# Performance work log

Hardware: AMD Instinct MI355X
Metric: run time of the kernel (lower is better)

## Reference

```python
import jax, jax.numpy as jnp
import numpy as np

NUM_RELATIONS = 8


def rgcn_conv(x, edge_index, edge_type, W, root, bias):
    """PyG RGCNConv (full weights, aggr='mean'): for each relation r, mean-aggregate
    W_r @ x_src over incoming edges of type r at each target node, sum over relations,
    then add root transform and bias."""
    N = x.shape[0]
    src, dst = edge_index[0], edge_index[1]
    # per-(relation, dst) edge counts for mean aggregation
    comb = edge_type * N + dst  # [E]
    cnt = jax.ops.segment_sum(jnp.ones(src.shape[0], x.dtype), comb,
                              num_segments=NUM_RELATIONS * N)  # [R*N]
    inv = jnp.where(cnt > 0, 1.0 / cnt, 0.0)
    # per-relation transformed features [R, N, H]
    xW = jnp.einsum('ni,rio->rno', x, W)
    # per-edge message, pre-scaled by 1/count for mean aggregation
    msg = xW[edge_type, src] * inv[comb][:, None]  # [E, H]
    agg = jax.ops.segment_sum(msg, dst, num_segments=N)  # [N, H]
    return agg + x @ root + bias


def setup_inputs() -> dict:
    key = jax.random.key(0)
    ks = jax.random.split(key, 9)
    N, E, D, H, C, R = 50000, 600000, 128, 128, 16, NUM_RELATIONS
    s1 = 1.0 / np.sqrt(D)
    s2 = 1.0 / np.sqrt(H)
    return {
        'x': jax.random.normal(ks[0], (N, D), jnp.float32),
        'edge_index': jax.random.randint(ks[1], (2, E), 0, N, jnp.int32),
        'edge_type': jax.random.randint(ks[2], (E,), 0, R, jnp.int32),
        'W1': jax.random.normal(ks[3], (R, D, H), jnp.float32) * s1,
        'root1': jax.random.normal(ks[4], (D, H), jnp.float32) * s1,
        'b1': jnp.zeros((H,), jnp.float32),
        'W2': jax.random.normal(ks[5], (R, H, H), jnp.float32) * s2,
        'root2': jax.random.normal(ks[6], (H, H), jnp.float32) * s2,
        'b2': jnp.zeros((H,), jnp.float32),
        'Wc': jax.random.normal(ks[7], (H, C), jnp.float32) * s2,
        'bc': jnp.zeros((C,), jnp.float32),
    }


def reference(x, edge_index, edge_type, W1, root1, b1, W2, root2, b2, Wc, bc):
    h = jax.nn.relu(rgcn_conv(x, edge_index, edge_type, W1, root1, b1))
    # dropout(p=0.2) is identity in eval mode
    embeddings = rgcn_conv(h, edge_index, edge_type, W2, root2, b2)
    out = embeddings @ Wc + bc
    return (out, embeddings)
```

## Files before the change

kernel.cpp:

```cpp
#include <hip/hip_runtime.h>

#define NREL 8

typedef __attribute__((ext_vector_type(8))) short bf16x8;
typedef __attribute__((ext_vector_type(4))) float f32x4;

__device__ inline ushort f2bf(float f)
{
    union { float f; unsigned u; } v; v.f = f;
    unsigned r = v.u + 0x7FFF + ((v.u >> 16) & 1);
    return (ushort)(r >> 16);
}

__device__ inline unsigned cvtpk(float lo, float hi)
{
    unsigned r;
    asm("v_cvt_pk_bf16_f32 %0, %1, %2" : "=v"(r) : "v"(lo), "v"(hi));
    return r;
}

__global__ __launch_bounds__(256) void zero16(float4* __restrict__ p, int n4)
{
    int i = blockIdx.x * 256 + threadIdx.x;
    int stride = gridDim.x * 256;
    for (; i < n4; i += stride) p[i] = make_float4(0.f, 0.f, 0.f, 0.f);
}

__global__ __launch_bounds__(256) void count_edges(
    const int* __restrict__ ei, const int* __restrict__ et,
    int* __restrict__ cnt, int E, int N)
{
    int e = blockIdx.x * 256 + threadIdx.x;
    if (e < E) {
        int d = ei[E + e];
        int r = et[e];
        atomicAdd(&cnt[r * N + d], 1);
    }
}

__global__ __launch_bounds__(256) void scan1f(
    const int* __restrict__ cnt, float* __restrict__ invc8,
    int* __restrict__ part, int* __restrict__ bsum, int N)
{
    __shared__ int tmp[256];
    int d = blockIdx.x * 256 + threadIdx.x;
    int s = 0;
    if (d < N) {
        #pragma unroll
        for (int r = 0; r < NREL; r++) {
            int c = cnt[r * N + d];
            s += c;
            invc8[(size_t)d * 8 + r] = (c > 0) ? 1.f / (float)c : 0.f;
        }
    }
    int v = s;
    tmp[threadIdx.x] = v;
    __syncthreads();
    for (int off = 1; off < 256; off <<= 1) {
        int t = (threadIdx.x >= off) ? tmp[threadIdx.x - off] : 0;
        __syncthreads();
        tmp[threadIdx.x] += t;
        __syncthreads();
    }
    if (d < N) part[d] = tmp[threadIdx.x] - v;
    if (threadIdx.x == 255) bsum[blockIdx.x] = tmp[255];
}

__global__ __launch_bounds__(1024) void scan2(int* __restrict__ bsum, int nb)
{
    __shared__ int tmp[1024];
    int tid = threadIdx.x;
    int v = (tid < nb) ? bsum[tid] : 0;
    tmp[tid] = v;
    __syncthreads();
    for (int off = 1; off < 1024; off <<= 1) {
        int t = (tid >= off) ? tmp[tid - off] : 0;
        __syncthreads();
        tmp[tid] += t;
        __syncthreads();
    }
    if (tid < nb) bsum[tid] = tmp[tid] - v;
}

__global__ __launch_bounds__(256) void scan3(
    const int* __restrict__ part, const int* __restrict__ bsum,
    int* __restrict__ rowptr, int* __restrict__ cursor, int n, int E)
{
    int i = blockIdx.x * 256 + threadIdx.x;
    if (i < n) {
        int v = part[i] + bsum[blockIdx.x];
        rowptr[i] = v;
        cursor[i] = v;
    }
    if (i == 0) rowptr[n] = E;
}

__global__ __launch_bounds__(256) void fill_csr(
    const int* __restrict__ ei, const int* __restrict__ et,
    int* __restrict__ cursor, int* __restrict__ spk, int E)
{
    int e = blockIdx.x * 256 + threadIdx.x;
    if (e < E) {
        int d = ei[E + e];
        int pos = atomicAdd(&cursor[d], 1);
        spk[pos] = (ei[e] << 8) | et[e];
    }
}

__global__ __launch_bounds__(256) void conv_x(
    const float* __restrict__ x, ushort* __restrict__ xb, int n4)
{
    int i = blockIdx.x * 256 + threadIdx.x;
    int stride = gridDim.x * 256;
    for (; i < n4; i += stride) {
        float4 v = ((const float4*)x)[i];
        ushort4 o;
        o.x = f2bf(v.x); o.y = f2bf(v.y); o.z = f2bf(v.z); o.w = f2bf(v.w);
        ((ushort4*)xb)[i] = o;
    }
}

__global__ __launch_bounds__(256) void conv_wfB(
    const float* __restrict__ W1, const float* __restrict__ root1,
    ushort* __restrict__ Wf1,
    const float* __restrict__ W2, const float* __restrict__ root2,
    ushort* __restrict__ Wf2)
{
    const float* W    = blockIdx.y ? W2 : W1;
    const float* root = blockIdx.y ? root2 : root1;
    ushort* Wf        = blockIdx.y ? Wf2 : Wf1;
    int i = blockIdx.x * 256 + threadIdx.x;
    if (i >= 128 * 1152) return;
    int f = i >> 9;
    int within = i & 511;
    int l = within >> 3;
    int j = within & 7;
    int rs = f >> 5;
    int kk = (f >> 3) & 3;
    int n  = f & 7;
    int col = (n << 4) | (l & 15);
    int kl  = kk * 32 + (l >> 4) * 8 + j;
    float v = (rs < 8) ? W[rs * 16384 + kl * 128 + col] : root[kl * 128 + col];
    Wf[i] = f2bf(v);
}

__global__ __launch_bounds__(1024, 8) void fused_layer(
    const ushort* __restrict__ Xb, const int* __restrict__ rowptr,
    const int* __restrict__ spk, const float* __restrict__ invc8,
    const ushort* __restrict__ Wf, const float* __restrict__ bias,
    float* __restrict__ Ofp, ushort* __restrict__ Obf, int N, int relu)
{
    __shared__ ushort lds[8 * 32 * 128];
    __shared__ f32x4 pscr[2][512];

    int wid  = threadIdx.x >> 6;
    int lane = threadIdx.x & 63;
    int blk0 = blockIdx.x * 32;
    int lane4 = lane << 2;

    #pragma unroll 1
    for (int rr = 0; rr < 2; rr++) {
        int lrow32 = wid * 2 + rr;
        int d = blk0 + lrow32;

        float2 a0 = {0.f, 0.f}, a1 = {0.f, 0.f}, a2 = {0.f, 0.f}, a3 = {0.f, 0.f};
        float2 a4 = {0.f, 0.f}, a5 = {0.f, 0.f}, a6 = {0.f, 0.f}, a7 = {0.f, 0.f};

        #define ROWLD(SP) \
            (*(const unsigned*)((const char*)Xb + (unsigned)((SP) | lane4)))
        #define CONSUME(P, U)                                               \
        {                                                                   \
            union { unsigned u; float f; } lo, hi;                          \
            lo.u = (U) << 16; hi.u = (U) & 0xFFFF0000u;                     \
            switch ((P) & 0xFF) {                                           \
                case 0: a0.x += lo.f; a0.y += hi.f; break;                  \
                case 1: a1.x += lo.f; a1.y += hi.f; break;                  \
                case 2: a2.x += lo.f; a2.y += hi.f; break;                  \
                case 3: a3.x += lo.f; a3.y += hi.f; break;                  \
                case 4: a4.x += lo.f; a4.y += hi.f; break;                  \
                case 5: a5.x += lo.f; a5.y += hi.f; break;                  \
                case 6: a6.x += lo.f; a6.y += hi.f; break;                  \
                default: a7.x += lo.f; a7.y += hi.f; break;                 \
            }                                                               \
        }

        if (d < N) {
            int beg = rowptr[d], end = rowptr[d + 1];
            int i = beg;
            for (; i + 8 <= end; i += 8) {
                int pk8 = spk[i + (lane & 7)];
                int p0 = __builtin_amdgcn_readlane(pk8, 0);
                int p1 = __builtin_amdgcn_readlane(pk8, 1);
                int p2 = __builtin_amdgcn_readlane(pk8, 2);
                int p3 = __builtin_amdgcn_readlane(pk8, 3);
                int p4 = __builtin_amdgcn_readlane(pk8, 4);
                int p5 = __builtin_amdgcn_readlane(pk8, 5);
                int p6 = __builtin_amdgcn_readlane(pk8, 6);
                int p7 = __builtin_amdgcn_readlane(pk8, 7);
                unsigned u0 = ROWLD(p0 & 0xFFFFFF00);
                unsigned u1 = ROWLD(p1 & 0xFFFFFF00);
                unsigned u2 = ROWLD(p2 & 0xFFFFFF00);
                unsigned u3 = ROWLD(p3 & 0xFFFFFF00);
                unsigned u4 = ROWLD(p4 & 0xFFFFFF00);
                unsigned u5 = ROWLD(p5 & 0xFFFFFF00);
                unsigned u6 = ROWLD(p6 & 0xFFFFFF00);
                unsigned u7 = ROWLD(p7 & 0xFFFFFF00);
                CONSUME(p0, u0);
                CONSUME(p1, u1);
                CONSUME(p2, u2);
                CONSUME(p3, u3);
                CONSUME(p4, u4);
                CONSUME(p5, u5);
                CONSUME(p6, u6);
                CONSUME(p7, u7);
            }
            for (; i + 4 <= end; i += 4) {
                int pk4 = spk[i + (lane & 3)];
                int p0 = __builtin_amdgcn_readlane(pk4, 0);
                int p1 = __builtin_amdgcn_readlane(pk4, 1);
                int p2 = __builtin_amdgcn_readlane(pk4, 2);
                int p3 = __builtin_amdgcn_readlane(pk4, 3);
                unsigned u0 = ROWLD(p0 & 0xFFFFFF00);
                unsigned u1 = ROWLD(p1 & 0xFFFFFF00);
                unsigned u2 = ROWLD(p2 & 0xFFFFFF00);
                unsigned u3 = ROWLD(p3 & 0xFFFFFF00);
                CONSUME(p0, u0);
                CONSUME(p1, u1);
                CONSUME(p2, u2);
                CONSUME(p3, u3);
            }
            for (; i < end; i++) {
                int p = __builtin_amdgcn_readfirstlane(spk[i]);
                unsigned u = ROWLD(p & 0xFFFFFF00);
                CONSUME(p, u);
            }
        }
        #undef CONSUME
        #undef ROWLD

        f32x4 iv0 = {0.f, 0.f, 0.f, 0.f}, iv1 = {0.f, 0.f, 0.f, 0.f};
        if (d < N) {
            iv0 = *(const f32x4*)&invc8[(size_t)d * 8];
            iv1 = *(const f32x4*)&invc8[(size_t)d * 8 + 4];
        }
        unsigned swz = (unsigned)(lrow32 & 7) << 4;
        char* rowbase = (char*)lds + (lrow32 << 8);
        unsigned wroff = (((unsigned)lane << 2)) ^ swz;
        #define WR2(R, A, IV)                                               \
        {                                                                   \
            unsigned pk = cvtpk(A.x * (IV), A.y * (IV));                    \
            *(unsigned*)(rowbase + (R << 13) + wroff) = pk;                 \
        }
        WR2(0, a0, iv0[0]) WR2(1, a1, iv0[1]) WR2(2, a2, iv0[2]) WR2(3, a3, iv0[3])
        WR2(4, a4, iv1[0]) WR2(5, a5, iv1[1]) WR2(6, a6, iv1[2]) WR2(7, a7, iv1[3])
        #undef WR2
    }
    __syncthreads();

    int lrow = lane & 15;
    int kgrp = lane >> 4;
    unsigned swzR = (unsigned)(lrow & 7) << 4;
    const bf16x8* Wf8 = (const bf16x8*)Wf;
    int n0    = wid & 7;
    int upper = wid >> 3;

    f32x4 acc0 = {0.f, 0.f, 0.f, 0.f};
    f32x4 acc1 = {0.f, 0.f, 0.f, 0.f};
    const char* ldsb = (const char*)lds;

    int rs0 = upper * 4;
    #pragma unroll 1
    for (int rs = rs0; rs < rs0 + 4; rs++) {
        const bf16x8* Bp = Wf8 + (size_t)rs * 2048 + (size_t)n0 * 64 + lane;
        bf16x8 b0 = Bp[0];
        bf16x8 b1 = Bp[512];
        bf16x8 b2 = Bp[1024];
        bf16x8 b3 = Bp[1536];
        const char* ab0 = ldsb + (rs << 13) + ((0 + lrow) << 8);
        const char* ab1 = ldsb + (rs << 13) + ((16 + lrow) << 8);
        {
            bf16x8 a0 = *(const bf16x8*)(ab0 + ((unsigned)(0 * 64 + kgrp * 16) ^ swzR));
            bf16x8 a1 = *(const bf16x8*)(ab0 + ((unsigned)(1 * 64 + kgrp * 16) ^ swzR));
            bf16x8 a2 = *(const bf16x8*)(ab0 + ((unsigned)(2 * 64 + kgrp * 16) ^ swzR));
            bf16x8 a3 = *(const bf16x8*)(ab0 + ((unsigned)(3 * 64 + kgrp * 16) ^ swzR));
            acc0 = __builtin_amdgcn_mfma_f32_16x16x32_bf16(a0, b0, acc0, 0, 0, 0);
            acc0 = __builtin_amdgcn_mfma_f32_16x16x32_bf16(a1, b1, acc0, 0, 0, 0);
            acc0 = __builtin_amdgcn_mfma_f32_16x16x32_bf16(a2, b2, acc0, 0, 0, 0);
            acc0 = __builtin_amdgcn_mfma_f32_16x16x32_bf16(a3, b3, acc0, 0, 0, 0);
        }
        {
            bf16x8 a0 = *(const bf16x8*)(ab1 + ((unsigned)(0 * 64 + kgrp * 16) ^ swzR));
            bf16x8 a1 = *(const bf16x8*)(ab1 + ((unsigned)(1 * 64 + kgrp * 16) ^ swzR));
            bf16x8 a2 = *(const bf16x8*)(ab1 + ((unsigned)(2 * 64 + kgrp * 16) ^ swzR));
            bf16x8 a3 = *(const bf16x8*)(ab1 + ((unsigned)(3 * 64 + kgrp * 16) ^ swzR));
            acc1 = __builtin_amdgcn_mfma_f32_16x16x32_bf16(a0, b0, acc1, 0, 0, 0);
            acc1 = __builtin_amdgcn_mfma_f32_16x16x32_bf16(a1, b1, acc1, 0, 0, 0);
            acc1 = __builtin_amdgcn_mfma_f32_16x16x32_bf16(a2, b2, acc1, 0, 0, 0);
            acc1 = __builtin_amdgcn_mfma_f32_16x16x32_bf16(a3, b3, acc1, 0, 0, 0);
        }
    }
    {
        int arow0 = blk0 + lrow;      if (arow0 >= N) arow0 = N - 1;
        int arow1 = blk0 + 16 + lrow; if (arow1 >= N) arow1 = N - 1;
        const ushort* A0 = Xb + (size_t)arow0 * 128;
        const ushort* A1 = Xb + (size_t)arow1 * 128;
        const bf16x8* Bp = Wf8 + (size_t)8 * 2048 + (size_t)n0 * 64 + lane;
        int kkb = upper * 2;
        bf16x8 b0 = Bp[(kkb + 0) * 512];
        bf16x8 b1 = Bp[(kkb + 1) * 512];
        bf16x8 a00 = *(const bf16x8*)(A0 + (kkb + 0) * 32 + kgrp * 8);
        bf16x8 a01 = *(const bf16x8*)(A0 + (kkb + 1) * 32 + kgrp * 8);
        bf16x8 a10 = *(const bf16x8*)(A1 + (kkb + 0) * 32 + kgrp * 8);
        bf16x8 a11 = *(const bf16x8*)(A1 + (kkb + 1) * 32 + kgrp * 8);
        acc0 = __builtin_amdgcn_mfma_f32_16x16x32_bf16(a00, b0, acc0, 0, 0, 0);
        acc0 = __builtin_amdgcn_mfma_f32_16x16x32_bf16(a01, b1, acc0, 0, 0, 0);
        acc1 = __builtin_amdgcn_mfma_f32_16x16x32_bf16(a10, b0, acc1, 0, 0, 0);
        acc1 = __builtin_amdgcn_mfma_f32_16x16x32_bf16(a11, b1, acc1, 0, 0, 0);
    }

    if (upper) {
        pscr[0][n0 * 64 + lane] = acc0;
        pscr[1][n0 * 64 + lane] = acc1;
    }
    __syncthreads();

    if (!upper) {
        f32x4 p0 = pscr[0][n0 * 64 + lane];
        f32x4 p1 = pscr[1][n0 * 64 + lane];
        int col = n0 * 16 + lrow;
        float bv = bias[col];
        #pragma unroll
        for (int rg = 0; rg < 2; rg++) {
            int row0 = blk0 + rg * 16 + kgrp * 4;
            f32x4 a = rg ? acc1 : acc0;
            f32x4 pp = rg ? p1 : p0;
            #pragma unroll
            for (int r = 0; r < 4; r++) {
                int row = row0 + r;
                if (row < N) {
                    float v = a[r] + pp[r] + bv;
                    if (relu) v = fmaxf(v, 0.f);
                    if (Ofp) Ofp[(size_t)row * 128 + col] = v;
                    if (Obf) Obf[(size_t)row * 128 + col] = f2bf(v);
                }
            }
        }
    }
}

__global__ __launch_bounds__(256) void classifier(
    const float* __restrict__ emb, const float* __restrict__ Wc,
    const float* __restrict__ bc, float* __restrict__ out, int N)
{
    int t = threadIdx.x;
    int c = t & 15;
    int n = blockIdx.x * 16 + (t >> 4);
    if (n >= N) return;
    const float* e = emb + (size_t)n * 128;
    float acc = bc[c];
    #pragma unroll 8
    for (int k = 0; k < 128; k++) acc += e[k] * Wc[k * 16 + c];
    out[(size_t)n * 16 + c] = acc;
}

static inline size_t align256(size_t x) { return (x + 255) & ~(size_t)255; }

extern "C" void kernel_launch(void* const* d_in, const int* in_sizes, int n_in,
                              void* d_out, int out_size, void* d_ws, size_t ws_size,
                              hipStream_t stream)
{
    const float* x     = (const float*)d_in[0];
    const int*   ei    = (const int*)d_in[1];
    const int*   et    = (const int*)d_in[2];
    const float* W1    = (const float*)d_in[3];
    const float* root1 = (const float*)d_in[4];
    const float* b1    = (const float*)d_in[5];
    const float* W2    = (const float*)d_in[6];
    const float* root2 = (const float*)d_in[7];
    const float* b2    = (const float*)d_in[8];
    const float* Wc    = (const float*)d_in[9];
    const float* bc    = (const float*)d_in[10];

    const int N = in_sizes[0] / 128;
    const int E = in_sizes[2];
    const int C = in_sizes[10];

    float* out = (float*)d_out;
    float* emb = out + (size_t)N * C;

    size_t cntB  = align256((size_t)NREL * N * sizeof(int));
    size_t rpB   = align256((size_t)(N + 1) * sizeof(int));
    size_t curB  = align256((size_t)N * sizeof(int));
    size_t bsB   = align256((size_t)1024 * sizeof(int));
    size_t invB  = align256((size_t)N * 8 * sizeof(float));
    size_t spkB  = align256((size_t)E * sizeof(int));
    size_t xbB   = align256((size_t)N * 128 * sizeof(ushort));
    size_t wtB   = align256((size_t)128 * 1152 * sizeof(ushort));

    char* p = (char*)d_ws;
    int*    cnt    = (int*)p;      p += cntB;
    int*    rowptr = (int*)p;      p += rpB;
    int*    cursor = (int*)p;      p += curB;
    int*    part   = (int*)p;      p += curB;
    int*    bsum   = (int*)p;      p += bsB;
    float*  invc8  = (float*)p;    p += invB;
    int*    spk    = (int*)p;      p += spkB;
    ushort* xb     = (ushort*)p;   p += xbB;
    ushort* hb     = (ushort*)p;   p += xbB;
    ushort* Wf1    = (ushort*)p;   p += wtB;
    ushort* Wf2    = (ushort*)p;

    dim3 blk(256);
    int gE    = (E + 255) / 256;
    int gN    = (N + 255) / 256;
    int gFus  = (N + 31) / 32;
    int gCls  = (N + 15) / 16;
    int gWt   = (128 * 1152 + 255) / 256;
    long long cnt4 = (long long)NREL * N / 4;
    int gZ = (int)((cnt4 + 255) / 256); if (gZ > 2048) gZ = 2048;
    int nx4 = N * 32;
    int gCx = (nx4 + 255) / 256; if (gCx > 2048) gCx = 2048;

    zero16<<<gZ, blk, 0, stream>>>((float4*)cnt, (int)cnt4);
    count_edges<<<gE, blk, 0, stream>>>(ei, et, cnt, E, N);
    scan1f<<<gN, blk, 0, stream>>>(cnt, invc8, part, bsum, N);
    scan2<<<1, 1024, 0, stream>>>(bsum, gN);
    scan3<<<gN, blk, 0, stream>>>(part, bsum, rowptr, cursor, N, E);
    fill_csr<<<gE, blk, 0, stream>>>(ei, et, cursor, spk, E);

    conv_x<<<gCx, blk, 0, stream>>>(x, xb, nx4);
    conv_wfB<<<dim3(gWt, 2), blk, 0, stream>>>(W1, root1, Wf1, W2, root2, Wf2);

    fused_layer<<<gFus, dim3(1024), 0, stream>>>(
        xb, rowptr, spk, invc8, Wf1, b1, nullptr, hb, N, 1);

    fused_layer<<<gFus, dim3(1024), 0, stream>>>(
        hb, rowptr, spk, invc8, Wf2, b2, emb, nullptr, N, 0);

    classifier<<<gCls, blk, 0, stream>>>(emb, Wc, bc, out, N);
}
```

Before: 261.1 us.

## Merge prep kernels, fuse classifier into layer two, prefetch edge indices

Three setup kernels (zeroing the count buffer, converting x to bf16, converting weights) are merged into one grid-stride kernel, which saves two launches. The classifier is fused into the second fused_layer epilogue: embeddings are staged in LDS and 512 threads compute the 16-class output, so emb is not re-read from global memory. The 8-edge gather loop also prefetches the next block of packed edge indices before the current one is consumed. The costs are an extra barrier plus reuse of the LDS buffer in layer two, and a longer serial prep kernel.

```diff
diff --git a/kernel.cpp b/kernel.cpp
--- a/kernel.cpp
+++ b/kernel.cpp
@@ -19,11 +19,47 @@
     return r;
 }
 
-__global__ __launch_bounds__(256) void zero16(float4* __restrict__ p, int n4)
-{
-    int i = blockIdx.x * 256 + threadIdx.x;
+__global__ __launch_bounds__(256) void prep1(
+    float4* __restrict__ cntz, int cnt4,
+    const float* __restrict__ x, ushort* __restrict__ xb, int nx4,
+    const float* __restrict__ W1, const float* __restrict__ root1,
+    ushort* __restrict__ Wf1,
+    const float* __restrict__ W2, const float* __restrict__ root2,
+    ushort* __restrict__ Wf2)
+{
+    int tid = blockIdx.x * 256 + threadIdx.x;
     int stride = gridDim.x * 256;
-    for (; i < n4; i += stride) p[i] = make_float4(0.f, 0.f, 0.f, 0.f);
+
+    for (int i = tid; i < cnt4; i += stride)
+        cntz[i] = make_float4(0.f, 0.f, 0.f, 0.f);
+
+    for (int i = tid; i < nx4; i += stride) {
+        float4 v = ((const float4*)x)[i];
+        ushort4 o;
+        o.x = f2bf(v.x); o.y = f2bf(v.y); o.z = f2bf(v.z); o.w = f2bf(v.w);
+        ((ushort4*)xb)[i] = o;
+    }
+
+    const int WFN = 128 * 1152;
+    for (int i = tid; i < 2 * WFN; i += stride) {
+        int half = (i >= WFN);
+        int j = half ? i - WFN : i;
+        const float* W    = half ? W2 : W1;
+        const float* root = half ? root2 : root1;
+        ushort* Wf        = half ? Wf2 : Wf1;
+        int f = j >> 9;
+        int within = j & 511;
+        int l = within >> 3;
+        int jj = within & 7;
+        int rs = f >> 5;
+        int kk = (f >> 3) & 3;
+        int n  = f & 7;
+        int col = (n << 4) | (l & 15);
+        int kl  = kk * 32 + (l >> 4) * 8 + jj;
+        float v = (rs < 8) ? W[rs * 16384 + kl * 128 + col]
+                           : root[kl * 128 + col];
+        Wf[j] = f2bf(v);
+    }
 }
 
 __global__ __launch_bounds__(256) void count_edges(
@@ -107,48 +143,13 @@
     }
 }
 
-__global__ __launch_bounds__(256) void conv_x(
-    const float* __restrict__ x, ushort* __restrict__ xb, int n4)
-{
-    int i = blockIdx.x * 256 + threadIdx.x;
-    int stride = gridDim.x * 256;
-    for (; i < n4; i += stride) {
-        float4 v = ((const float4*)x)[i];
-        ushort4 o;
-        o.x = f2bf(v.x); o.y = f2bf(v.y); o.z = f2bf(v.z); o.w = f2bf(v.w);
-        ((ushort4*)xb)[i] = o;
-    }
-}
-
-__global__ __launch_bounds__(256) void conv_wfB(
-    const float* __restrict__ W1, const float* __restrict__ root1,
-    ushort* __restrict__ Wf1,
-    const float* __restrict__ W2, const float* __restrict__ root2,
-    ushort* __restrict__ Wf2)
-{
-    const float* W    = blockIdx.y ? W2 : W1;
-    const float* root = blockIdx.y ? root2 : root1;
-    ushort* Wf        = blockIdx.y ? Wf2 : Wf1;
-    int i = blockIdx.x * 256 + threadIdx.x;
-    if (i >= 128 * 1152) return;
-    int f = i >> 9;
-    int within = i & 511;
-    int l = within >> 3;
-    int j = within & 7;
-    int rs = f >> 5;
-    int kk = (f >> 3) & 3;
-    int n  = f & 7;
-    int col = (n << 4) | (l & 15);
-    int kl  = kk * 32 + (l >> 4) * 8 + j;
-    float v = (rs < 8) ? W[rs * 16384 + kl * 128 + col] : root[kl * 128 + col];
-    Wf[i] = f2bf(v);
-}
-
 __global__ __launch_bounds__(1024, 8) void fused_layer(
     const ushort* __restrict__ Xb, const int* __restrict__ rowptr,
     const int* __restrict__ spk, const float* __restrict__ invc8,
     const ushort* __restrict__ Wf, const float* __restrict__ bias,
-    float* __restrict__ Ofp, ushort* __restrict__ Obf, int N, int relu)
+    float* __restrict__ Ofp, ushort* __restrict__ Obf,
+    const float* __restrict__ Wc, const float* __restrict__ bc,
+    float* __restrict__ outC, int N, int relu)
 {
     __shared__ ushort lds[8 * 32 * 128];
     __shared__ f32x4 pscr[2][512];
@@ -187,16 +188,19 @@
         if (d < N) {
             int beg = rowptr[d], end = rowptr[d + 1];
             int i = beg;
-            for (; i + 8 <= end; i += 8) {
-                int pk8 = spk[i + (lane & 7)];
-                int p0 = __builtin_amdgcn_readlane(pk8, 0);
-                int p1 = __builtin_amdgcn_readlane(pk8, 1);
-                int p2 = __builtin_amdgcn_readlane(pk8, 2);
-                int p3 = __builtin_amdgcn_readlane(pk8, 3);
-                int p4 = __builtin_amdgcn_readlane(pk8, 4);
-                int p5 = __builtin_amdgcn_readlane(pk8, 5);
-                int p6 = __builtin_amdgcn_readlane(pk8, 6);
-                int p7 = __builtin_amdgcn_readlane(pk8, 7);
+            int pk8 = (i + 8 <= end) ? spk[i + (lane & 7)] : 0;
+            for (; i + 8 <= end; ) {
+                int cur = pk8;
+                i += 8;
+                if (i + 8 <= end) pk8 = spk[i + (lane & 7)];
+                int p0 = __builtin_amdgcn_readlane(cur, 0);
+                int p1 = __builtin_amdgcn_readlane(cur, 1);
+                int p2 = __builtin_amdgcn_readlane(cur, 2);
+                int p3 = __builtin_amdgcn_readlane(cur, 3);
+                int p4 = __builtin_amdgcn_readlane(cur, 4);
+                int p5 = __builtin_amdgcn_readlane(cur, 5);
+                int p6 = __builtin_amdgcn_readlane(cur, 6);
+                int p7 = __builtin_amdgcn_readlane(cur, 7);
                 unsigned u0 = ROWLD(p0 & 0xFFFFFF00);
                 unsigned u1 = ROWLD(p1 & 0xFFFFFF00);
                 unsigned u2 = ROWLD(p2 & 0xFFFFFF00);
@@ -329,38 +333,40 @@
         f32x4 p1 = pscr[1][n0 * 64 + lane];
         int col = n0 * 16 + lrow;
         float bv = bias[col];
+        float* embt = (float*)lds;
         #pragma unroll
         for (int rg = 0; rg < 2; rg++) {
-            int row0 = blk0 + rg * 16 + kgrp * 4;
+            int lrowb = rg * 16 + kgrp * 4;
             f32x4 a = rg ? acc1 : acc0;
             f32x4 pp = rg ? p1 : p0;
             #pragma unroll
             for (int r = 0; r < 4; r++) {
-                int row = row0 + r;
+                int row = blk0 + lrowb + r;
+                float v = a[r] + pp[r] + bv;
+                if (relu) v = fmaxf(v, 0.f);
+                if (outC) embt[(lrowb + r) * 128 + col] = v;
                 if (row < N) {
-                    float v = a[r] + pp[r] + bv;
-                    if (relu) v = fmaxf(v, 0.f);
                     if (Ofp) Ofp[(size_t)row * 128 + col] = v;
                     if (Obf) Obf[(size_t)row * 128 + col] = f2bf(v);
                 }
             }
         }
     }
-}
-
-__global__ __launch_bounds__(256) void classifier(
-    const float* __restrict__ emb, const float* __restrict__ Wc,
-    const float* __restrict__ bc, float* __restrict__ out, int N)
-{
-    int t = threadIdx.x;
-    int c = t & 15;
-    int n = blockIdx.x * 16 + (t >> 4);
-    if (n >= N) return;
-    const float* e = emb + (size_t)n * 128;
-    float acc = bc[c];
-    #pragma unroll 8
-    for (int k = 0; k < 128; k++) acc += e[k] * Wc[k * 16 + c];
-    out[(size_t)n * 16 + c] = acc;
+
+    if (outC) {
+        __syncthreads();
+        int t = threadIdx.x;
+        if (t < 512) {
+            int row = t >> 4;
+            int c = t & 15;
+            const float* er = (const float*)lds + row * 128;
+            float acc2 = bc[c];
+            #pragma unroll 8
+            for (int k = 0; k < 128; k++) acc2 += er[k] * Wc[k * 16 + c];
+            int grow = blk0 + row;
+            if (grow < N) outC[(size_t)grow * 16 + c] = acc2;
+        }
+    }
 }
 
 static inline size_t align256(size_t x) { return (x + 255) & ~(size_t)255; }
@@ -414,28 +420,24 @@
     int gE    = (E + 255) / 256;
     int gN    = (N + 255) / 256;
     int gFus  = (N + 31) / 32;
-    int gCls  = (N + 15) / 16;
-    int gWt   = (128 * 1152 + 255) / 256;
     long long cnt4 = (long long)NREL * N / 4;
-    int gZ = (int)((cnt4 + 255) / 256); if (gZ > 2048) gZ = 2048;
     int nx4 = N * 32;
-    int gCx = (nx4 + 255) / 256; if (gCx > 2048) gCx = 2048;
-
-    zero16<<<gZ, blk, 0, stream>>>((float4*)cnt, (int)cnt4);
+
+    prep1<<<2048, blk, 0, stream>>>((float4*)cnt, (int)cnt4,
+                                    x, xb, nx4,
+                                    W1, root1, Wf1, W2, root2, Wf2);
+
     count_edges<<<gE, blk, 0, stream>>>(ei, et, cnt, E, N);
     scan1f<<<gN, blk, 0, stream>>>(cnt, invc8, part, bsum, N);
     scan2<<<1, 1024, 0, stream>>>(bsum, gN);
     scan3<<<gN, blk, 0, stream>>>(part, bsum, rowptr, cursor, N, E);
     fill_csr<<<gE, blk, 0, stream>>>(ei, et, cursor, spk, E);
 
-    conv_x<<<gCx, blk, 0, stream>>>(x, xb, nx4);
-    conv_wfB<<<dim3(gWt, 2), blk, 0, stream>>>(W1, root1, Wf1, W2, root2, Wf2);
-
     fused_layer<<<gFus, dim3(1024), 0, stream>>>(
-        xb, rowptr, spk, invc8, Wf1, b1, nullptr, hb, N, 1);
+        xb, rowptr, spk, invc8, Wf1, b1, nullptr, hb,
+        nullptr, nullptr, nullptr, N, 1);
 
     fused_layer<<<gFus, dim3(1024), 0, stream>>>(
-        hb, rowptr, spk, invc8, Wf2, b2, emb, nullptr, N, 0);
-
-    classifier<<<gCls, blk, 0, stream>>>(emb, Wc, bc, out, N);
-}
+        hb, rowptr, spk, invc8, Wf2, b2, emb, nullptr,
+        Wc, bc, out, N, 0);
+}
```

Result: faster. 236.4 us (-9.4%).
